# Optimization experiments

Hardware: AMD Instinct MI355X
Metric: run time of the kernel (lower is better)

Reference implementation:

```python
import jax, jax.numpy as jnp
import numpy as np

N, DIM, H, HD = 2048, 1280, 16, 80

def _rotate_half(x):
    x1, x2 = x[..., :x.shape[-1] // 2], x[..., x.shape[-1] // 2:]
    return jnp.concatenate((-x2, x1), axis=-1)

def setup_inputs() -> dict:
    key = jax.random.key(0)
    ks = jax.random.split(key, 6)
    hidden_states = jax.random.normal(ks[0], (N, DIM), dtype=jnp.float32)
    cu_seqlens = jnp.array([0, N // 2, N], dtype=jnp.int32)  # 2 packed segments
    # rotary embeddings: half-dim inverse frequencies, duplicated to head_dim
    inv_freq = 1.0 / (10000.0 ** (np.arange(0, HD // 2, dtype=np.float32) * 2.0 / HD))
    pos = np.arange(N, dtype=np.float32) % (N // 2)  # positions restart per segment
    freqs = pos[:, None] * inv_freq[None, :]           # [N, HD/2]
    emb = jnp.asarray(np.concatenate([freqs, freqs], axis=-1))  # [N, HD]
    cos, sin = jnp.cos(emb), jnp.sin(emb)
    Wqkv = jax.random.normal(ks[1], (DIM, 3 * DIM), dtype=jnp.float32) * (DIM ** -0.5)
    bqkv = jax.random.normal(ks[2], (3 * DIM,), dtype=jnp.float32) * 0.02
    Wproj = jax.random.normal(ks[3], (DIM, DIM), dtype=jnp.float32) * (DIM ** -0.5)
    bproj = jax.random.normal(ks[4], (DIM,), dtype=jnp.float32) * 0.02
    return {"hidden_states": hidden_states, "cu_seqlens": cu_seqlens,
            "cos": cos, "sin": sin, "Wqkv": Wqkv, "bqkv": bqkv,
            "Wproj": Wproj, "bproj": bproj}

def reference(hidden_states, cu_seqlens, cos, sin, Wqkv, bqkv, Wproj, bproj):
    n = hidden_states.shape[0]
    scale = HD ** -0.5
    qkv = (hidden_states @ Wqkv + bqkv).reshape(n, 3, H, HD)
    q, k, v = qkv[:, 0], qkv[:, 1], qkv[:, 2]           # each [N, H, HD]
    # RoPE (fp32), cos/sin broadcast over heads: [N, 1, HD]
    c, s = cos[:, None, :], sin[:, None, :]
    q = q * c + _rotate_half(q) * s
    k = k * c + _rotate_half(k) * s
    # block-diagonal varlen mask from cu_seqlens (per-segment full attention)
    seg_id = jnp.searchsorted(cu_seqlens, jnp.arange(n), side='right')  # [N]
    mask = seg_id[:, None] == seg_id[None, :]                           # [N, N]
    scores = jnp.einsum('qhd,khd->hqk', q, k) * scale                   # [H, N, N]
    scores = jnp.where(mask[None], scores, -jnp.inf)
    attn = jax.nn.softmax(scores.astype(jnp.float32), axis=-1).astype(q.dtype)
    out = jnp.einsum('hqk,khd->qhd', attn, v).reshape(n, H * HD)        # [N, DIM]
    return out @ Wproj + bproj
```

## Files before the change

### kernel.cpp

```cpp
#include <hip/hip_runtime.h>
#include <hip/hip_bf16.h>

constexpr int N_TOK  = 2048;
constexpr int DIM    = 1280;
constexpr int NHEAD  = 16;
constexpr int HD     = 80;
constexpr int QKV_N  = 3 * DIM;

using bf16 = __hip_bfloat16;
typedef __attribute__((ext_vector_type(4)))  float f32x4;
typedef __attribute__((ext_vector_type(16))) float f32x16;
typedef __attribute__((ext_vector_type(8)))  short short8;

__device__ __forceinline__ float b2f(bf16 x) { return __bfloat162float(x); }
__device__ __forceinline__ bf16  f2b(float x) { return __float2bfloat16(x); }

__device__ __forceinline__ unsigned int pk2(float a, float b) {
  __align__(4) bf16 t[2] = {f2b(a), f2b(b)};
  return *reinterpret_cast<unsigned int*>(t);
}

typedef const __attribute__((address_space(1))) unsigned int* gas_u32;
typedef __attribute__((address_space(3))) unsigned int* las_u32;
__device__ __forceinline__ void gload_lds16(const void* g, void* l) {
  __builtin_amdgcn_global_load_lds((gas_u32)g, (las_u32)l, 16, 0, 0);
}

__device__ __forceinline__ void transpose_body(const float* __restrict__ W,
                                               bf16* __restrict__ WT, int K, int N) {
  __shared__ float tile[32][33];
  const int n0 = blockIdx.x * 32, k0 = blockIdx.y * 32;
  const int tc = threadIdx.x & 31, tr = threadIdx.x >> 5;
#pragma unroll
  for (int r = tr; r < 32; r += 8)
    tile[r][tc] = W[(size_t)(k0 + r) * N + n0 + tc];
  __syncthreads();
#pragma unroll
  for (int r = tr; r < 32; r += 8)
    WT[(size_t)(n0 + r) * K + k0 + tc] = f2b(tile[tc][r]);
}

__global__ __launch_bounds__(256)
void prep_kernel(const float* __restrict__ hs, bf16* __restrict__ hsb,
                 const float* __restrict__ Wqkv, bf16* __restrict__ WqkvT,
                 const float* __restrict__ Wproj, bf16* __restrict__ WprojT) {
  if (blockIdx.z == 0) {
    const int bid = blockIdx.y * gridDim.x + blockIdx.x;
    if (bid >= (N_TOK * DIM) / 2048) return;
    const int i = bid * 2048 + threadIdx.x * 8;
    const float4 a = *reinterpret_cast<const float4*>(hs + i);
    const float4 b = *reinterpret_cast<const float4*>(hs + i + 4);
    __align__(16) bf16 w[8] = {f2b(a.x), f2b(a.y), f2b(a.z), f2b(a.w),
                               f2b(b.x), f2b(b.y), f2b(b.z), f2b(b.w)};
    *reinterpret_cast<short8*>(hsb + i) = *reinterpret_cast<const short8*>(w);
  } else if (blockIdx.z == 1) {
    transpose_body(Wqkv, WqkvT, DIM, QKV_N);
  } else {
    if (blockIdx.x >= DIM / 32) return;
    transpose_body(Wproj, WprojT, DIM, DIM);
  }
}

template <int OBF>
__global__ __launch_bounds__(256)
void mfma_gemm(const bf16* __restrict__ A, const bf16* __restrict__ BT,
               const float* __restrict__ bias, void* __restrict__ C,
               int M, int N, int K) {
  __shared__ bf16 As[128 * 64];
  __shared__ bf16 Bs[128 * 64];
  const int tid = threadIdx.x;
  const int wid = tid >> 6, lane = tid & 63;
  const int lm = lane & 15, kg = lane >> 4;
  const int wm = (wid >> 1) * 64, wn = (wid & 1) * 64;
  const int m0 = blockIdx.y * 128, n0 = blockIdx.x * 128;

  const int srow = lane >> 3;
  const int sblk = (lane & 7) ^ srow;

  f32x4 acc[4][4];
#pragma unroll
  for (int i = 0; i < 4; ++i)
#pragma unroll
    for (int j = 0; j < 4; ++j) acc[i][j] = (f32x4){0.f, 0.f, 0.f, 0.f};

  for (int k0 = 0; k0 < K; k0 += 64) {
#pragma unroll
    for (int i = 0; i < 4; ++i) {
      const int slot = i * 4 + wid;
      const int row = slot * 8 + srow;
      gload_lds16(A + (size_t)(m0 + row) * K + k0 + sblk * 8, &As[slot * 512]);
      gload_lds16(BT + (size_t)(n0 + row) * K + k0 + sblk * 8, &Bs[slot * 512]);
    }
    __syncthreads();

#pragma unroll
    for (int kh = 0; kh < 2; ++kh) {
      short8 af[4], bfr[4];
#pragma unroll
      for (int t = 0; t < 4; ++t) {
        const int ar = wm + t * 16 + lm;
        af[t] = *reinterpret_cast<const short8*>(
            &As[ar * 64 + ((kh * 4 + kg) ^ (ar & 7)) * 8]);
        const int br = wn + t * 16 + lm;
        bfr[t] = *reinterpret_cast<const short8*>(
            &Bs[br * 64 + ((kh * 4 + kg) ^ (br & 7)) * 8]);
      }
#pragma unroll
      for (int mi = 0; mi < 4; ++mi)
#pragma unroll
        for (int ni = 0; ni < 4; ++ni)
          acc[mi][ni] = __builtin_amdgcn_mfma_f32_16x16x32_bf16(
              af[mi], bfr[ni], acc[mi][ni], 0, 0, 0);
    }
    __syncthreads();
  }

#pragma unroll
  for (int mi = 0; mi < 4; ++mi) {
#pragma unroll
    for (int ni = 0; ni < 4; ++ni) {
      const int col = n0 + wn + ni * 16 + lm;
      const float bv = bias[col];
#pragma unroll
      for (int r = 0; r < 4; ++r) {
        const int row = m0 + wm + mi * 16 + kg * 4 + r;
        const float v = acc[mi][ni][r] + bv;
        if constexpr (OBF)
          ((bf16*)C)[(size_t)row * N + col] = f2b(v);
        else
          ((float*)C)[(size_t)row * N + col] = v;
      }
    }
  }
}

__global__ void rope_kernel(bf16* __restrict__ qkv, const float* __restrict__ cosb,
                            const float* __restrict__ sinb) {
  constexpr int HALF = HD / 2;
  int idx = blockIdx.x * blockDim.x + threadIdx.x;
  int n     = idx / (2 * NHEAD * HALF);
  int rem   = idx % (2 * NHEAD * HALF);
  int which = rem / (NHEAD * HALF);
  int rem2  = rem % (NHEAD * HALF);
  int h     = rem2 / HALF;
  int d     = rem2 % HALF;
  size_t base = (size_t)n * QKV_N + which * DIM + h * HD;
  float x1 = b2f(qkv[base + d]), x2 = b2f(qkv[base + d + HALF]);
  float c1 = cosb[n * HD + d], c2 = cosb[n * HD + d + HALF];
  float s1 = sinb[n * HD + d], s2 = sinb[n * HD + d + HALF];
  qkv[base + d]        = f2b(x1 * c1 - x2 * s1);
  qkv[base + d + HALF] = f2b(x2 * c2 + x1 * s2);
}

constexpr int KC   = 64;
constexpr int KSTR = 104;
constexpr int VSTR = 88;
constexpr int VROWS = 96;

__global__ __launch_bounds__(256)
void attn_mfma_kernel(const bf16* __restrict__ qkv, const int* __restrict__ cu,
                      bf16* __restrict__ out, int nseg) {
  __shared__ bf16 Ks[2][KC * KSTR];
  __shared__ bf16 Vt[VROWS * VSTR];

  const int p = blockIdx.x;
  const int lidx = (p & 7) * (gridDim.x >> 3) + (p >> 3);
  const int xt  = lidx & 15;
  const int seg = (lidx >> 4) % nseg;
  const int h   = (lidx >> 4) / nseg;

  const int s0 = cu[seg], s1 = cu[seg + 1];
  if (s0 + xt * 128 >= s1) return;

  const int tid  = threadIdx.x;
  const int wid  = tid >> 6, lane = tid & 63;
  const int l31  = lane & 31;
  const int half = lane >> 5;
  const float scale = 0.11180339887498949f;

  const int qrow = s0 + xt * 128 + wid * 32 + l31;

  if (tid < 176) {
    int r = 80 + tid / 11, sl = tid % 11;
    *reinterpret_cast<short8*>(&Vt[r * VSTR + sl * 8]) =
        (short8){0, 0, 0, 0, 0, 0, 0, 0};
  }

  short8 qa[5];
#pragma unroll
  for (int ck = 0; ck < 5; ++ck) {
    const int dbase = ck * 16 + half * 8;
    qa[ck] = (qrow < s1)
        ? *reinterpret_cast<const short8*>(qkv + (size_t)qrow * QKV_N + h * HD + dbase)
        : (short8){0, 0, 0, 0, 0, 0, 0, 0};
  }

  short8 kreg[3], vreg[4];
  const int vgrp = tid / 10, vsl = tid % 10;
  auto issueK = [&](int c) {
    const int k0 = s0 + c * KC;
#pragma unroll
    for (int t = 0; t < 3; ++t) {
      const int s = tid + t * 256;
      if (s < 640) {
        const int r = min(k0 + s / 10, s1 - 1);
        kreg[t] = *reinterpret_cast<const short8*>(
            qkv + (size_t)r * QKV_N + DIM + h * HD + (s % 10) * 8);
      }
    }
  };
  auto commitK = [&](int buf) {
#pragma unroll
    for (int t = 0; t < 3; ++t) {
      const int s = tid + t * 256;
      if (s < 640)
        *reinterpret_cast<short8*>(&Ks[buf][(s / 10) * KSTR + (s % 10) * 8]) =
            kreg[t];
    }
  };
  auto issueV = [&](int c) {
    if (tid < 160) {
      const int k0 = s0 + c * KC;
#pragma unroll
      for (int e = 0; e < 4; ++e) {
        const int r = min(k0 + vgrp * 4 + e, s1 - 1);
        vreg[e] = *reinterpret_cast<const short8*>(
            qkv + (size_t)r * QKV_N + 2 * DIM + h * HD + vsl * 8);
      }
    }
  };
  auto commitV = [&]() {
    if (tid < 160) {
      const int r0 = vgrp * 4;
      const int swz = (vsl & 7) << 3;
#pragma unroll
      for (int de = 0; de < 8; ++de) {
        __align__(8) bf16 w[4] = {reinterpret_cast<const bf16*>(&vreg[0])[de],
                                  reinterpret_cast<const bf16*>(&vreg[1])[de],
                                  reinterpret_cast<const bf16*>(&vreg[2])[de],
                                  reinterpret_cast<const bf16*>(&vreg[3])[de]};
        *reinterpret_cast<uint2*>(&Vt[(vsl * 8 + de) * VSTR + (r0 ^ swz)]) =
            *reinterpret_cast<const uint2*>(w);
      }
    }
  };

  f32x16 oacc[3];
#pragma unroll
  for (int dt = 0; dt < 3; ++dt)
#pragma unroll
    for (int r = 0; r < 16; ++r) oacc[dt][r] = 0.f;
  float m = -1e30f, l = 0.f;
  const int nch = (s1 - s0 + KC - 1) / KC;

  issueK(0);
  issueV(0);
  commitK(0);
  if (nch > 1) issueK(1);
  __syncthreads();

  for (int c = 0; c < nch; ++c) {
    const int cur = c & 1;
    const int nk = min(KC, s1 - (s0 + c * KC));

    commitV();

    f32x16 sc[2];
    __builtin_amdgcn_s_setprio(1);
#pragma unroll
    for (int kt = 0; kt < 2; ++kt) {
#pragma unroll
      for (int r = 0; r < 16; ++r) sc[kt][r] = 0.f;
#pragma unroll
      for (int ck = 0; ck < 5; ++ck) {
        short8 ka = *reinterpret_cast<const short8*>(
            &Ks[cur][(kt * 32 + l31) * KSTR + ck * 16 + half * 8]);
        sc[kt] = __builtin_amdgcn_mfma_f32_32x32x16_bf16(ka, qa[ck], sc[kt], 0, 0, 0);
      }
    }
    __builtin_amdgcn_s_setprio(0);

    if (c + 1 < nch) {
      commitK(cur ^ 1);
      issueV(c + 1);
    }
    if (c + 2 < nch) issueK(c + 2);

#pragma unroll
    for (int kt = 0; kt < 2; ++kt)
#pragma unroll
      for (int r = 0; r < 16; ++r) sc[kt][r] *= scale;
    if (nk < KC) {
#pragma unroll
      for (int kt = 0; kt < 2; ++kt)
#pragma unroll
        for (int r = 0; r < 16; ++r) {
          const int key = kt * 32 + (r & 3) + 8 * (r >> 2) + 4 * half;
          if (key >= nk) sc[kt][r] = -1e30f;
        }
    }
    float rml = sc[0][0];
#pragma unroll
    for (int kt = 0; kt < 2; ++kt)
#pragma unroll
      for (int r = 0; r < 16; ++r)
        if (kt | r) rml = fmaxf(rml, sc[kt][r]);
    if (!__all(rml - m <= 8.0f)) {
      float rm = fmaxf(rml, __shfl_xor(rml, 32));
      const float mnew = fmaxf(m, rm);
      const float fs = __expf(m - mnew);
      m = mnew;
      l *= fs;
#pragma unroll
      for (int dt = 0; dt < 3; ++dt)
#pragma unroll
        for (int r = 0; r < 16; ++r) oacc[dt][r] *= fs;
    }
#pragma unroll
    for (int kt = 0; kt < 2; ++kt)
#pragma unroll
      for (int r = 0; r < 16; ++r) {
        sc[kt][r] = __expf(sc[kt][r] - m);
        l += sc[kt][r];
      }

    unsigned int pbw[4][4];
#pragma unroll
    for (int kt = 0; kt < 2; ++kt) {
      unsigned int w[8];
#pragma unroll
      for (int i = 0; i < 8; ++i) w[i] = pk2(sc[kt][2 * i], sc[kt][2 * i + 1]);
#pragma unroll
      for (int kc2 = 0; kc2 < 2; ++kc2) {
        auto r02 = __builtin_amdgcn_permlane32_swap(w[4 * kc2 + 0],
                                                    w[4 * kc2 + 2], false, false);
        auto r13 = __builtin_amdgcn_permlane32_swap(w[4 * kc2 + 1],
                                                    w[4 * kc2 + 3], false, false);
        pbw[kt * 2 + kc2][0] = r02[0];
        pbw[kt * 2 + kc2][1] = r13[0];
        pbw[kt * 2 + kc2][2] = r02[1];
        pbw[kt * 2 + kc2][3] = r13[1];
      }
    }

    __syncthreads();

    __builtin_amdgcn_s_setprio(1);
#pragma unroll
    for (int kc = 0; kc < 4; ++kc) {
      short8 pb = *reinterpret_cast<const short8*>(&pbw[kc][0]);
#pragma unroll
      for (int dt = 0; dt < 3; ++dt) {
        const int d = dt * 32 + l31;
        short8 va = *reinterpret_cast<const short8*>(
            &Vt[d * VSTR + ((kc * 16 + half * 8) ^ (((d >> 3) & 7) << 3))]);
        oacc[dt] = __builtin_amdgcn_mfma_f32_32x32x16_bf16(va, pb, oacc[dt], 0, 0, 0);
      }
    }
    __builtin_amdgcn_s_setprio(0);

    __syncthreads();
  }

  l += __shfl_xor(l, 32);
  if (qrow < s1) {
    const float inv = 1.f / l;
    bf16* op = out + (size_t)qrow * DIM + h * HD;
#pragma unroll
    for (int dt = 0; dt < 3; ++dt) {
#pragma unroll
      for (int g = 0; g < 4; ++g) {
        const int d = dt * 32 + g * 8 + half * 4;
        if (d < HD) {
          __align__(8) bf16 w[4] = {f2b(oacc[dt][g * 4 + 0] * inv),
                                    f2b(oacc[dt][g * 4 + 1] * inv),
                                    f2b(oacc[dt][g * 4 + 2] * inv),
                                    f2b(oacc[dt][g * 4 + 3] * inv)};
          *reinterpret_cast<uint2*>(op + d) = *reinterpret_cast<const uint2*>(w);
        }
      }
    }
  }
}

extern "C" void kernel_launch(void* const* d_in, const int* in_sizes, int n_in,
                              void* d_out, int out_size, void* d_ws, size_t ws_size,
                              hipStream_t stream) {
  const float* hs    = (const float*)d_in[0];
  const int*   cu    = (const int*)d_in[1];
  const float* cosb  = (const float*)d_in[2];
  const float* sinb  = (const float*)d_in[3];
  const float* Wqkv  = (const float*)d_in[4];
  const float* bqkv  = (const float*)d_in[5];
  const float* Wproj = (const float*)d_in[6];
  const float* bproj = (const float*)d_in[7];

  bf16* qkv      = (bf16*)d_ws;
  bf16* attn_out = qkv + (size_t)N_TOK * QKV_N;
  bf16* WqkvT    = attn_out + (size_t)N_TOK * DIM;
  bf16* WprojT   = WqkvT + (size_t)QKV_N * DIM;
  bf16* hsb      = WprojT + (size_t)DIM * DIM;

  prep_kernel<<<dim3(QKV_N / 32, DIM / 32, 3), 256, 0, stream>>>(
      hs, hsb, Wqkv, WqkvT, Wproj, WprojT);

  mfma_gemm<1><<<dim3(QKV_N / 128, N_TOK / 128), 256, 0, stream>>>(
      hsb, WqkvT, bqkv, qkv, N_TOK, QKV_N, DIM);

  rope_kernel<<<(N_TOK * 2 * NHEAD * (HD / 2)) / 256, 256, 0, stream>>>(
      qkv, cosb, sinb);

  int nseg = in_sizes[1] - 1;
  int nblk = (N_TOK / 128) * nseg * NHEAD;
  attn_mfma_kernel<<<nblk, 256, 0, stream>>>(qkv, cu, attn_out, nseg);

  mfma_gemm<0><<<dim3(DIM / 128, N_TOK / 128), 256, 0, stream>>>(
      attn_out, WprojT, bproj, d_out, N_TOK, DIM, DIM);
}
```

Measured before the change: 113.8 us.

## Double-buffer V tile in attention and vectorize RoPE kernel

```diff
diff --git a/kernel.cpp b/kernel.cpp
--- a/kernel.cpp
+++ b/kernel.cpp
@@ -134,22 +134,43 @@
   }
 }
 
-__global__ void rope_kernel(bf16* __restrict__ qkv, const float* __restrict__ cosb,
-                            const float* __restrict__ sinb) {
-  constexpr int HALF = HD / 2;
-  int idx = blockIdx.x * blockDim.x + threadIdx.x;
-  int n     = idx / (2 * NHEAD * HALF);
-  int rem   = idx % (2 * NHEAD * HALF);
-  int which = rem / (NHEAD * HALF);
-  int rem2  = rem % (NHEAD * HALF);
-  int h     = rem2 / HALF;
-  int d     = rem2 % HALF;
-  size_t base = (size_t)n * QKV_N + which * DIM + h * HD;
-  float x1 = b2f(qkv[base + d]), x2 = b2f(qkv[base + d + HALF]);
-  float c1 = cosb[n * HD + d], c2 = cosb[n * HD + d + HALF];
-  float s1 = sinb[n * HD + d], s2 = sinb[n * HD + d + HALF];
-  qkv[base + d]        = f2b(x1 * c1 - x2 * s1);
-  qkv[base + d + HALF] = f2b(x2 * c2 + x1 * s2);
+__global__ __launch_bounds__(256)
+void rope_kernel(bf16* __restrict__ qkv, const float* __restrict__ cosb,
+                 const float* __restrict__ sinb) {
+  const int idx  = blockIdx.x * 256 + threadIdx.x;
+  const int d0   = (idx % 5) * 8;
+  const int h    = (idx / 5) % NHEAD;
+  const int whch = (idx / (5 * NHEAD)) % 2;
+  const int n    = idx / (10 * NHEAD);
+  const size_t base = (size_t)n * QKV_N + whch * DIM + h * HD;
+
+  short8 a = *reinterpret_cast<const short8*>(qkv + base + d0);
+  short8 b = *reinterpret_cast<const short8*>(qkv + base + 40 + d0);
+  const float4 c0 = *reinterpret_cast<const float4*>(cosb + n * HD + d0);
+  const float4 c1 = *reinterpret_cast<const float4*>(cosb + n * HD + d0 + 4);
+  const float4 c2 = *reinterpret_cast<const float4*>(cosb + n * HD + 40 + d0);
+  const float4 c3 = *reinterpret_cast<const float4*>(cosb + n * HD + 44 + d0);
+  const float4 s0 = *reinterpret_cast<const float4*>(sinb + n * HD + d0);
+  const float4 s1 = *reinterpret_cast<const float4*>(sinb + n * HD + d0 + 4);
+  const float4 s2 = *reinterpret_cast<const float4*>(sinb + n * HD + 40 + d0);
+  const float4 s3 = *reinterpret_cast<const float4*>(sinb + n * HD + 44 + d0);
+  const float* cl = &c0.x;
+  float cc1[8] = {c0.x, c0.y, c0.z, c0.w, c1.x, c1.y, c1.z, c1.w};
+  float cc2[8] = {c2.x, c2.y, c2.z, c2.w, c3.x, c3.y, c3.z, c3.w};
+  float ss1[8] = {s0.x, s0.y, s0.z, s0.w, s1.x, s1.y, s1.z, s1.w};
+  float ss2[8] = {s2.x, s2.y, s2.z, s2.w, s3.x, s3.y, s3.z, s3.w};
+  (void)cl;
+
+  __align__(16) bf16 o1[8], o2[8];
+#pragma unroll
+  for (int e = 0; e < 8; ++e) {
+    const float x1 = b2f(reinterpret_cast<const bf16*>(&a)[e]);
+    const float x2 = b2f(reinterpret_cast<const bf16*>(&b)[e]);
+    o1[e] = f2b(x1 * cc1[e] - x2 * ss1[e]);
+    o2[e] = f2b(x2 * cc2[e] + x1 * ss2[e]);
+  }
+  *reinterpret_cast<short8*>(qkv + base + d0)      = *reinterpret_cast<const short8*>(o1);
+  *reinterpret_cast<short8*>(qkv + base + 40 + d0) = *reinterpret_cast<const short8*>(o2);
 }
 
 constexpr int KC   = 64;
@@ -161,7 +182,7 @@
 void attn_mfma_kernel(const bf16* __restrict__ qkv, const int* __restrict__ cu,
                       bf16* __restrict__ out, int nseg) {
   __shared__ bf16 Ks[2][KC * KSTR];
-  __shared__ bf16 Vt[VROWS * VSTR];
+  __shared__ bf16 Vt[2][VROWS * VSTR];
 
   const int p = blockIdx.x;
   const int lidx = (p & 7) * (gridDim.x >> 3) + (p >> 3);
@@ -180,10 +201,15 @@
 
   const int qrow = s0 + xt * 128 + wid * 32 + l31;
 
-  if (tid < 176) {
-    int r = 80 + tid / 11, sl = tid % 11;
-    *reinterpret_cast<short8*>(&Vt[r * VSTR + sl * 8]) =
-        (short8){0, 0, 0, 0, 0, 0, 0, 0};
+#pragma unroll
+  for (int t = 0; t < 2; ++t) {
+    const int s = tid + t * 256;
+    if (s < 352) {
+      const int b = s / 176, rem = s % 176;
+      const int r = 80 + rem / 11, sl = rem % 11;
+      *reinterpret_cast<short8*>(&Vt[b][r * VSTR + sl * 8]) =
+          (short8){0, 0, 0, 0, 0, 0, 0, 0};
+    }
   }
 
   short8 qa[5];
@@ -229,7 +255,7 @@
       }
     }
   };
-  auto commitV = [&]() {
+  auto commitV = [&](int buf) {
     if (tid < 160) {
       const int r0 = vgrp * 4;
       const int swz = (vsl & 7) << 3;
@@ -239,7 +265,7 @@
                                   reinterpret_cast<const bf16*>(&vreg[1])[de],
                                   reinterpret_cast<const bf16*>(&vreg[2])[de],
                                   reinterpret_cast<const bf16*>(&vreg[3])[de]};
-        *reinterpret_cast<uint2*>(&Vt[(vsl * 8 + de) * VSTR + (r0 ^ swz)]) =
+        *reinterpret_cast<uint2*>(&Vt[buf][(vsl * 8 + de) * VSTR + (r0 ^ swz)]) =
             *reinterpret_cast<const uint2*>(w);
       }
     }
@@ -256,14 +282,16 @@
   issueK(0);
   issueV(0);
   commitK(0);
-  if (nch > 1) issueK(1);
+  commitV(0);
+  if (nch > 1) {
+    issueK(1);
+    issueV(1);
+  }
   __syncthreads();
 
   for (int c = 0; c < nch; ++c) {
     const int cur = c & 1;
     const int nk = min(KC, s1 - (s0 + c * KC));
-
-    commitV();
 
     f32x16 sc[2];
     __builtin_amdgcn_s_setprio(1);
@@ -282,9 +310,12 @@
 
     if (c + 1 < nch) {
       commitK(cur ^ 1);
-      issueV(c + 1);
-    }
-    if (c + 2 < nch) issueK(c + 2);
+      commitV(cur ^ 1);
+    }
+    if (c + 2 < nch) {
+      issueK(c + 2);
+      issueV(c + 2);
+    }
 
 #pragma unroll
     for (int kt = 0; kt < 2; ++kt)
@@ -343,8 +374,6 @@
       }
     }
 
-    __syncthreads();
-
     __builtin_amdgcn_s_setprio(1);
 #pragma unroll
     for (int kc = 0; kc < 4; ++kc) {
@@ -353,7 +382,7 @@
       for (int dt = 0; dt < 3; ++dt) {
         const int d = dt * 32 + l31;
         short8 va = *reinterpret_cast<const short8*>(
-            &Vt[d * VSTR + ((kc * 16 + half * 8) ^ (((d >> 3) & 7) << 3))]);
+            &Vt[cur][d * VSTR + ((kc * 16 + half * 8) ^ (((d >> 3) & 7) << 3))]);
         oacc[dt] = __builtin_amdgcn_mfma_f32_32x32x16_bf16(va, pb, oacc[dt], 0, 0, 0);
       }
     }
@@ -407,7 +436,7 @@
   mfma_gemm<1><<<dim3(QKV_N / 128, N_TOK / 128), 256, 0, stream>>>(
       hsb, WqkvT, bqkv, qkv, N_TOK, QKV_N, DIM);
 
-  rope_kernel<<<(N_TOK * 2 * NHEAD * (HD / 2)) / 256, 256, 0, stream>>>(
+  rope_kernel<<<(N_TOK * 2 * NHEAD * 5) / 256, 256, 0, stream>>>(
       qkv, cosb, sinb);
 
   int nseg = in_sizes[1] - 1;
```

New measurement: 111.4 us. 2.1% less time.
